# Optimization experiments

Measured on AMD Instinct MI355X. Metric: run time of the kernel, lower is better.

## Reference

```python
import jax, jax.numpy as jnp
import numpy as np

# Marching-tetrahedra lookup tables (identical to the torch module).
_TRI_TABLE = np.array([
    [-1,-1,-1,-1,-1,-1],[1,0,2,-1,-1,-1],[4,0,3,-1,-1,-1],[1,4,2,1,3,4],
    [3,1,5,-1,-1,-1],[2,3,0,2,5,3],[1,4,0,1,5,4],[4,2,5,-1,-1,-1],
    [4,5,2,-1,-1,-1],[4,1,0,4,5,1],[3,2,0,3,5,2],[1,3,5,-1,-1,-1],
    [4,1,2,4,3,1],[3,0,4,-1,-1,-1],[2,0,1,-1,-1,-1],[-1,-1,-1,-1,-1,-1]], dtype=np.int64)
_NUM_TRI = np.array([0,1,1,2,1,2,2,1,1,2,2,1,2,1,1,0], dtype=np.int64)
_BASE_EDGES = np.array([0,1,0,2,0,3,1,2,1,3,2,3], dtype=np.int64)
_NUM_TETS = np.array([0,1,1,3,1,3,3,3,1,3,3,3,3,3,3,1], dtype=np.int64)
_TET_TABLE = np.array([
    [-1,-1,-1,-1,-1,-1,-1,-1,-1,-1,-1,-1],[0,4,5,6,-1,-1,-1,-1,-1,-1,-1,-1],
    [1,4,8,7,-1,-1,-1,-1,-1,-1,-1,-1],[7,1,8,6,5,1,7,6,5,0,1,6],
    [2,5,7,9,-1,-1,-1,-1,-1,-1,-1,-1],[4,0,6,7,9,0,7,6,7,0,9,2],
    [4,1,9,8,5,1,9,4,5,1,2,9],[6,0,1,2,8,6,1,2,9,6,8,2],
    [3,6,9,8,-1,-1,-1,-1,-1,-1,-1,-1],[5,0,4,8,5,0,8,3,5,8,9,3],
    [1,4,7,3,4,7,6,3,9,6,7,3],[0,1,5,3,5,1,9,3,5,1,7,9],
    [5,2,3,7,3,6,5,8,3,5,7,8],[0,4,7,8,0,3,8,7,0,3,7,2],
    [4,1,2,3,4,3,2,5,4,3,5,6],[0,1,2,3,-1,-1,-1,-1,-1,-1,-1,-1]], dtype=np.int64)


def _precompute(n_verts, sdf, tet, thickness):
    """Integer / no_grad half of DMTet.__call__ (dynamic shapes -> host numpy)."""
    sdf = np.asarray(sdf)
    tet = np.asarray(tet).astype(np.int64)
    th = float(np.asarray(thickness).reshape(-1)[0])
    occ = (sdf > 0) & (sdf <= th)                      # [N]
    occ_f = occ[tet]                                   # [F,4]
    occ_sum = occ_f.sum(-1)
    valid = (occ_sum > 0) & (occ_sum < 4)
    vt = tet[valid]                                    # [V,4] surface tets
    edges = vt[:, _BASE_EDGES].reshape(-1, 2)          # [V*6,2]
    edges = np.sort(edges, axis=1)                     # == sort_edges
    uniq, inv = np.unique(edges, axis=0, return_inverse=True)
    inv = inv.reshape(-1)
    mask_e = occ[uniq].sum(-1) == 1                    # crossing edges
    mapping = np.full(uniq.shape[0], -1, dtype=np.int64)
    mapping[mask_e] = np.arange(int(mask_e.sum()), dtype=np.int64)
    idx_map = mapping[inv].reshape(-1, 6)              # [V,6]
    interp_v = uniq[mask_e]                            # [E,2]
    ti = (occ_f[valid].astype(np.int64) * np.array([1, 2, 4, 8])).sum(-1)  # tetindex
    nt = _NUM_TRI[ti]
    f1 = np.take_along_axis(idx_map[nt == 1], _TRI_TABLE[ti[nt == 1]][:, :3], axis=1).reshape(-1, 3)
    f2 = np.take_along_axis(idx_map[nt == 2], _TRI_TABLE[ti[nt == 2]][:, :6], axis=1).reshape(-1, 3)
    faces = np.concatenate([f1, f2], axis=0)
    ntt = _NUM_TETS[ti]
    tve = np.concatenate([vt, idx_map + n_verts], axis=1)  # [V,10]: 4 verts + 6 edge-verts
    t1 = np.take_along_axis(tve[ntt == 1], _TET_TABLE[ti[ntt == 1]][:, :4], axis=1).reshape(-1, 4)
    t3 = np.take_along_axis(tve[ntt == 3], _TET_TABLE[ti[ntt == 3]][:, :12], axis=1).reshape(-1, 4)
    inner = tet[occ_sum == 4]
    all_tets = np.concatenate([t1, t3, inner], axis=0)
    all_unique, inv2 = np.unique(all_tets.reshape(-1), return_inverse=True)
    tets_tetmesh = inv2.reshape(-1, 4)
    return interp_v, faces, all_unique, tets_tetmesh


def _interp(pos, sdf, th, interp_v, all_unique_tets):
    """Differentiable half: edge interpolation + gather of tetmesh verts."""
    e = pos[interp_v.reshape(-1)].reshape(-1, 2, 3)    # [E,2,3]
    s = sdf[interp_v.reshape(-1)].reshape(-1, 2, 1)    # [E,2,1]
    both_pos = (s[:, 0, 0] > 0) & (s[:, 1, 0] > 0)
    s = jnp.where(both_pos[:, None, None], s - th, s)  # shift band edges
    s = s * jnp.array([1.0, -1.0], dtype=s.dtype)[None, :, None]  # negate 2nd
    denom = s.sum(axis=1, keepdims=True)
    w = jnp.flip(s, axis=1) / denom                    # linear interp weights
    verts = (e * w).sum(axis=1)                        # [E,3]
    all_verts = jnp.concatenate([pos, verts], axis=0)
    verts_tetmesh = all_verts[all_unique_tets]
    return verts, verts_tetmesh


def setup_inputs() -> dict:
    key = jax.random.key(0)
    k1, k2, k3, k4 = jax.random.split(key, 4)
    N, F = 400000, 2000000
    pos_nx3 = jax.random.normal(k1, (N, 3), dtype=jnp.float32)
    sdf_n = jax.random.normal(k2, (N,), dtype=jnp.float32)
    tet_fx4 = jax.random.randint(k3, (F, 4), 0, N, dtype=jnp.int32)
    thickness = jax.random.uniform(k4, (1,), dtype=jnp.float32, minval=0.3, maxval=0.8)
    return {"pos_nx3": pos_nx3, "sdf_n": sdf_n, "tet_fx4": tet_fx4, "thickness": thickness}


def reference(pos_nx3, sdf_n, tet_fx4, thickness):
    interp_v, faces, all_unique, tets_tm = _precompute(pos_nx3.shape[0], sdf_n, tet_fx4, thickness)
    verts, verts_tetmesh = _interp(pos_nx3, sdf_n, thickness[0], jnp.asarray(interp_v), jnp.asarray(all_unique))
    return verts, jnp.asarray(faces), verts_tetmesh, jnp.asarray(tets_tm)
```

## Files before the change

kernel.cpp:

```cpp
#include <hip/hip_runtime.h>
#include <stdint.h>

typedef unsigned int u32;
typedef unsigned long long u64;

__device__ __constant__ int c_TRI[16][6] = {
 {-1,-1,-1,-1,-1,-1},{1,0,2,-1,-1,-1},{4,0,3,-1,-1,-1},{1,4,2,1,3,4},
 {3,1,5,-1,-1,-1},{2,3,0,2,5,3},{1,4,0,1,5,4},{4,2,5,-1,-1,-1},
 {4,5,2,-1,-1,-1},{4,1,0,4,5,1},{3,2,0,3,5,2},{1,3,5,-1,-1,-1},
 {4,1,2,4,3,1},{3,0,4,-1,-1,-1},{2,0,1,-1,-1,-1},{-1,-1,-1,-1,-1,-1}};
__device__ __constant__ int c_NTRI[16] = {0,1,1,2,1,2,2,1,1,2,2,1,2,1,1,0};
__device__ __constant__ int c_NTET[16] = {0,1,1,3,1,3,3,3,1,3,3,3,3,3,3,1};
__device__ __constant__ int c_TET[16][12] = {
 {-1,-1,-1,-1,-1,-1,-1,-1,-1,-1,-1,-1},{0,4,5,6,-1,-1,-1,-1,-1,-1,-1,-1},
 {1,4,8,7,-1,-1,-1,-1,-1,-1,-1,-1},{7,1,8,6,5,1,7,6,5,0,1,6},
 {2,5,7,9,-1,-1,-1,-1,-1,-1,-1,-1},{4,0,6,7,9,0,7,6,7,0,9,2},
 {4,1,9,8,5,1,9,4,5,1,2,9},{6,0,1,2,8,6,1,2,9,6,8,2},
 {3,6,9,8,-1,-1,-1,-1,-1,-1,-1,-1},{5,0,4,8,5,0,8,3,5,8,9,3},
 {1,4,7,3,4,7,6,3,9,6,7,3},{0,1,5,3,5,1,9,3,5,1,7,9},
 {5,2,3,7,3,6,5,8,3,5,7,8},{0,4,7,8,0,3,8,7,0,3,7,2},
 {4,1,2,3,4,3,2,5,4,3,5,6},{0,1,2,3,-1,-1,-1,-1,-1,-1,-1,-1}};
__device__ __constant__ int c_EV[12] = {0,1,0,2,0,3,1,2,1,3,2,3};

#define GSLOOP(i,n) for (long long i = (long long)blockIdx.x*blockDim.x + threadIdx.x; \
                         i < (long long)(n); i += (long long)gridDim.x*blockDim.x)

__global__ __launch_bounds__(256) void k_scan1(u32* data, u32* partials,
                                               const u32* hdr, int nslot, u32 nmax) {
  __shared__ u32 lds[2048];
  __shared__ u32 tsum[256];
  u32 n = (nslot >= 0) ? hdr[nslot] : nmax;
  u32 base = blockIdx.x * 2048u;
  for (int k = threadIdx.x; k < 2048; k += 256) {
    u32 i = base + (u32)k;
    lds[k] = (i < n) ? data[i] : 0u;
  }
  __syncthreads();
  u32 o = threadIdx.x * 8u;
  u32 run = 0; u32 loc[8];
  #pragma unroll
  for (int j = 0; j < 8; j++) { loc[j] = run; run += lds[o + j]; }
  tsum[threadIdx.x] = run;
  __syncthreads();
  for (int off = 1; off < 256; off <<= 1) {
    u32 v = tsum[threadIdx.x];
    u32 add = (threadIdx.x >= (u32)off) ? tsum[threadIdx.x - off] : 0u;
    __syncthreads();
    tsum[threadIdx.x] = v + add;
    __syncthreads();
  }
  u32 texc = (threadIdx.x == 0) ? 0u : tsum[threadIdx.x - 1];
  #pragma unroll
  for (int j = 0; j < 8; j++) {
    u32 i = base + o + (u32)j;
    if (i < n) data[i] = texc + loc[j];
  }
  if (threadIdx.x == 0) partials[blockIdx.x] = tsum[255];
}

__global__ __launch_bounds__(1024) void k_scan2(u32* partials, const u32* hdr, int nslot,
                                                u32 nmax, u32* hdrw, int tslot) {
  __shared__ u32 lds[8192];
  __shared__ u32 tsum[1024];
  u32 n = (nslot >= 0) ? hdr[nslot] : nmax;
  u32 nb = (n + 2047u) / 2048u;
  for (int k = threadIdx.x; k < 8192; k += 1024) lds[k] = ((u32)k < nb) ? partials[k] : 0u;
  __syncthreads();
  u32 o = threadIdx.x * 8u;
  u32 run = 0; u32 loc[8];
  #pragma unroll
  for (int j = 0; j < 8; j++) { loc[j] = run; run += lds[o + j]; }
  tsum[threadIdx.x] = run;
  __syncthreads();
  for (int off = 1; off < 1024; off <<= 1) {
    u32 v = tsum[threadIdx.x];
    u32 add = (threadIdx.x >= (u32)off) ? tsum[threadIdx.x - off] : 0u;
    __syncthreads();
    tsum[threadIdx.x] = v + add;
    __syncthreads();
  }
  u32 texc = (threadIdx.x == 0) ? 0u : tsum[threadIdx.x - 1];
  #pragma unroll
  for (int j = 0; j < 8; j++) { u32 k = o + (u32)j; if (k < nb) partials[k] = texc + loc[j]; }
  if (threadIdx.x == 0 && tslot >= 0) hdrw[tslot] = tsum[1023];
}

__global__ __launch_bounds__(256) void k_scan3(u32* data, const u32* partials,
                                               const u32* hdr, int nslot, u32 nmax) {
  u32 n = (nslot >= 0) ? hdr[nslot] : nmax;
  u32 base = blockIdx.x * 2048u;
  if (base >= n || blockIdx.x == 0) return;
  u32 add = partials[blockIdx.x];
  if (add == 0) return;
  for (int k = threadIdx.x; k < 2048; k += 256) {
    u32 i = base + (u32)k;
    if (i < n) data[i] += add;
  }
}

__global__ void k_zero32(u32* p, long long n) { GSLOOP(i, n) p[i] = 0u; }
__global__ void k_zero_hdr(u32* p, const u32* hdr, int slot, u32 extra) {
  long long n = (long long)hdr[slot] + extra;
  GSLOOP(i, n) p[i] = 0u;
}
__global__ void k_copy32(const u32* s, u32* d, long long n) { GSLOOP(i, n) d[i] = s[i]; }

__global__ void k_occ(const float* sdf, const float* th, unsigned char* occ, int N) {
  float t = th[0];
  GSLOOP(i, N) { float s = sdf[i]; occ[i] = (s > 0.f && s <= t) ? 1 : 0; }
}

__global__ void k_ti(const int* tet, const unsigned char* occ, unsigned char* ti,
                     u32* S1, long long F) {
  GSLOOP(f, F) {
    int v0 = tet[4*f], v1 = tet[4*f+1], v2 = tet[4*f+2], v3 = tet[4*f+3];
    int b = (int)occ[v0] | ((int)occ[v1] << 1) | ((int)occ[v2] << 2) | ((int)occ[v3] << 3);
    ti[f] = (unsigned char)b;
    S1[f] = (b != 0 && b != 15) ? 1u : 0u;
  }
}

__global__ void k_compact_valid(const u32* S1, const unsigned char* ti, u32* vidx, long long F) {
  GSLOOP(f, F) { int b = ti[f]; if (b != 0 && b != 15) vidx[S1[f]] = (u32)f; }
}

__global__ void k_hist(const int* tet, const u32* vidx, const u32* hdr, u32* hist) {
  u32 V = hdr[0];
  GSLOOP(t, V) {
    long long f = vidx[t];
    int v[4] = { tet[4*f], tet[4*f+1], tet[4*f+2], tet[4*f+3] };
    #pragma unroll
    for (int e = 0; e < 6; e++) {
      int a = v[c_EV[2*e]], b = v[c_EV[2*e+1]];
      int mn = a < b ? a : b;
      atomicAdd(&hist[mn], 1u);
    }
  }
}

__global__ void k_scatter(const int* tet, const u32* vidx, const u32* hdr,
                          u32* cursor, u64* keys, int SB, int OB) {
  u32 V = hdr[0];
  GSLOOP(t, V) {
    long long f = vidx[t];
    int v[4] = { tet[4*f], tet[4*f+1], tet[4*f+2], tet[4*f+3] };
    #pragma unroll
    for (int e = 0; e < 6; e++) {
      int a = v[c_EV[2*e]], b = v[c_EV[2*e+1]];
      int mn = a < b ? a : b, mx = a < b ? b : a;
      u32 p = atomicAdd(&cursor[mn], 1u);
      u64 key = ((((u64)(u32)mn << SB) | (u64)(u32)mx) << OB) | (u64)(6ull * t + e);
      keys[p] = key;
    }
  }
}

template<int KMAX>
__device__ __forceinline__ void bitonic_lane(u64& val, int lane) {
  #pragma unroll
  for (int k = 2; k <= KMAX; k <<= 1) {
    #pragma unroll
    for (int j = k >> 1; j > 0; j >>= 1) {
      u64 other = __shfl_xor(val, j, 64);
      bool keepmin = ((lane & k) == 0) == ((lane & j) == 0);
      bool smaller = val < other;
      val = (keepmin == smaller) ? val : other;
    }
  }
}

__global__ __launch_bounds__(256) void k_bsort(const u32* off, u64* keys, int N) {
  int lane = threadIdx.x & 63;
  long long wid = ((long long)blockIdx.x * blockDim.x + threadIdx.x) >> 6;
  long long nw  = ((long long)gridDim.x * blockDim.x) >> 6;
  for (long long v = wid; v < N; v += nw) {
    u32 s = off[v], e = off[v + 1];
    u32 cnt = e - s;
    if (cnt <= 1) continue;
    if (cnt <= 64) {
      u64 val = (lane < (int)cnt) ? keys[s + lane] : ~0ull;
      if      (cnt <= 2)  bitonic_lane<2>(val, lane);
      else if (cnt <= 4)  bitonic_lane<4>(val, lane);
      else if (cnt <= 8)  bitonic_lane<8>(val, lane);
      else if (cnt <= 16) bitonic_lane<16>(val, lane);
      else if (cnt <= 32) bitonic_lane<32>(val, lane);
      else                bitonic_lane<64>(val, lane);
      if (lane < (int)cnt) keys[s + lane] = val;
    } else if (cnt <= 256) {
      u64 vals[4];
      #pragma unroll
      for (int r = 0; r < 4; r++) {
        int idx = r * 64 + lane;
        vals[r] = (idx < (int)cnt) ? keys[s + idx] : ~0ull;
      }
      #pragma unroll
      for (int k = 2; k <= 256; k <<= 1) {
        #pragma unroll
        for (int j = 128; j > 0; j >>= 1) {
          if (j >= k) continue;
          if (j >= 64) {
            int rj = j >> 6;
            #pragma unroll
            for (int r = 0; r < 4; r++) {
              int pr = r ^ rj;
              if (pr > r) {
                int i0 = r * 64 + lane;
                bool keepmin = ((i0 & k) == 0);
                u64 a = vals[r], b = vals[pr];
                u64 mn = a < b ? a : b, mx = a < b ? b : a;
                vals[r]  = keepmin ? mn : mx;
                vals[pr] = keepmin ? mx : mn;
              }
            }
          } else {
            #pragma unroll
            for (int r = 0; r < 4; r++) {
              int i0 = r * 64 + lane;
              u64 other = __shfl_xor(vals[r], j, 64);
              bool keepmin = ((i0 & k) == 0) == ((i0 & j) == 0);
              bool smaller = vals[r] < other;
              vals[r] = (keepmin == smaller) ? vals[r] : other;
            }
          }
        }
      }
      #pragma unroll
      for (int r = 0; r < 4; r++) {
        int idx = r * 64 + lane;
        if (idx < (int)cnt) keys[s + idx] = vals[r];
      }
    } else if (lane == 0) {
      for (u32 i = s + 1; i < e; i++) {
        u64 kk = keys[i]; u32 j = i;
        while (j > s && keys[j - 1] > kk) { keys[j] = keys[j - 1]; j--; }
        keys[j] = kk;
      }
    }
  }
}

__global__ void k_uflag(const u64* keys, u32* Big, const u32* hdr, int OB) {
  u32 E = hdr[1];
  GSLOOP(i, E) Big[i] = (i == 0 || (keys[i] >> OB) != (keys[i - 1] >> OB)) ? 1u : 0u;
}

__global__ void k_ucompact(const u64* keys, const u32* Big, u64* uk, const u32* hdr, int OB) {
  u32 E = hdr[1];
  GSLOOP(i, E) {
    u64 k = keys[i] >> OB;
    if (i == 0 || k != (keys[i - 1] >> OB)) uk[Big[i]] = k;
  }
}

__global__ void k_cflag(const u64* uk, const unsigned char* occ, u32* Cf, const u32* hdr, int SB) {
  u32 U = hdr[2];
  u64 mask = ((u64)1 << SB) - 1;
  GSLOOP(u, U) {
    u64 k = uk[u]; int a = (int)(k >> SB), b = (int)(k & mask);
    Cf[u] = (((int)occ[a] + (int)occ[b]) == 1) ? 1u : 0u;
  }
}

__global__ void k_mapping(const u64* uk, const unsigned char* occ, int* Cf,
                          u32* hdr, int N, int SB) {
  if (blockIdx.x == 0 && threadIdx.x == 0) hdr[10] = (u32)N + hdr[3];
  u32 U = hdr[2];
  u64 mask = ((u64)1 << SB) - 1;
  GSLOOP(u, U) {
    u64 k = uk[u]; int a = (int)(k >> SB), b = (int)(k & mask);
    bool c = (((int)occ[a] + (int)occ[b]) == 1);
    Cf[u] = c ? Cf[u] : -1;
  }
}

__global__ void k_idxscatter(const u64* keys, const u32* Big, const int* mapping,
                             int* idx_map, const u32* hdr, int OB) {
  u32 E = hdr[1];
  u64 omask = ((u64)1 << OB) - 1;
  GSLOOP(i, E) {
    u64 k = keys[i];
    bool flag = (i == 0) || ((k >> OB) != (keys[i - 1] >> OB));
    u32 rank = flag ? Big[i] : Big[i] - 1u;
    idx_map[(u32)(k & omask)] = mapping[rank];
  }
}

__global__ void k_interp(const u64* uk, const int* mapping, const float* pos,
                         const float* sdf, const float* th, float* out, const u32* hdr, int SB) {
  u32 U = hdr[2];
  float t = th[0];
  u64 mask = ((u64)1 << SB) - 1;
  GSLOOP(u, U) {
    int m = mapping[u]; if (m < 0) continue;
    u64 k = uk[u]; int a = (int)(k >> SB), b = (int)(k & mask);
    float s0 = sdf[a], s1 = sdf[b];
    if (s0 > 0.f && s1 > 0.f) { s0 = __fsub_rn(s0, t); s1 = __fsub_rn(s1, t); }
    float denom = __fadd_rn(s0, -s1);
    float w0 = __fdiv_rn(-s1, denom);
    float w1 = __fdiv_rn(s0, denom);
    long long base = 3ll * m;
    #pragma unroll
    for (int kk = 0; kk < 3; kk++)
      out[base + kk] = __fadd_rn(__fmul_rn(pos[3ll*a + kk], w0), __fmul_rn(pos[3ll*b + kk], w1));
  }
}

__global__ void k_pred_faces(const unsigned char* ti, u32* S1, u32* S2, long long F) {
  GSLOOP(f, F) {
    int b = ti[f]; bool valid = (b != 0 && b != 15); int nt = c_NTRI[b];
    S1[f] = (valid && nt == 1) ? 1u : 0u;
    S2[f] = (valid && nt == 2) ? 1u : 0u;
  }
}

__global__ void k_faces(const u32* vidx, const unsigned char* ti, const int* idx_map,
                        const u32* S1, const u32* S2, float* out, const u32* hdr) {
  u32 V = hdr[0];
  unsigned long long fo = 3ull * hdr[3];
  u32 Nf1 = hdr[4];
  GSLOOP(t, V) {
    u32 f = vidx[t]; int b = ti[f]; int nt = c_NTRI[b];
    if (nt == 1) {
      unsigned long long base = fo + 3ull * S1[f];
      for (int k = 0; k < 3; k++) out[base + k] = (float)idx_map[6*t + c_TRI[b][k]];
    } else {
      unsigned long long base = fo + 3ull * Nf1 + 6ull * S2[f];
      for (int k = 0; k < 6; k++) out[base + k] = (float)idx_map[6*t + c_TRI[b][k]];
    }
  }
}

__global__ void k_pred_tets(const unsigned char* ti, u32* S1, u32* S2, u32* S3, long long F) {
  GSLOOP(f, F) {
    int b = ti[f]; bool valid = (b != 0 && b != 15); int ntt = c_NTET[b];
    S1[f] = (valid && ntt == 1) ? 1u : 0u;
    S2[f] = (valid && ntt == 3) ? 1u : 0u;
    S3[f] = (b == 15) ? 1u : 0u;
  }
}

__global__ void k_tets_valid(const int* tet, const u32* vidx, const unsigned char* ti,
                             const int* idx_map, const u32* S1, const u32* S2,
                             int* at, const u32* hdr, int N) {
  u32 V = hdr[0]; u32 Nt1 = hdr[6];
  GSLOOP(t, V) {
    u32 f = vidx[t]; int b = ti[f];
    int tv[10];
    for (int k = 0; k < 4; k++) tv[k] = tet[4ll*f + k];
    for (int j = 0; j < 6; j++) tv[4 + j] = idx_map[6*t + j] + N;
    int ntt = c_NTET[b];
    if (ntt == 1) {
      long long base = 4ll * S1[f];
      for (int k = 0; k < 4; k++) at[base + k] = tv[c_TET[b][k]];
    } else {
      long long base = 4ll * Nt1 + 12ll * S2[f];
      for (int k = 0; k < 12; k++) at[base + k] = tv[c_TET[b][k]];
    }
  }
}

__global__ void k_tets_inner(const int* tet, const unsigned char* ti, const u32* S3,
                             int* at, const u32* hdr, long long F) {
  long long base0 = 4ll * hdr[6] + 12ll * hdr[7];
  GSLOOP(f, F) {
    if (ti[f] == 15) {
      long long base = base0 + 4ll * S3[f];
      for (int k = 0; k < 4; k++) at[base + k] = tet[4*f + k];
    }
  }
}

__global__ void k_mark(const int* at, u32* Big, const u32* hdr) {
  long long NA = 4ll * hdr[6] + 12ll * hdr[7] + 4ll * hdr[8];
  GSLOOP(i, NA) Big[at[i]] = 1u;
}

__global__ void k_vtm(const u32* Big, const float* pos, float* out, const u32* hdr, int N) {
  u32 R = hdr[10], NU = hdr[9];
  unsigned long long vtm = 3ull * hdr[3] + 3ull * (hdr[4] + 2u * hdr[5]);
  GSLOOP(v, R) {
    u32 r = Big[v];
    u32 nx = (v + 1 < (long long)R) ? Big[v + 1] : NU;
    if (nx > r) {
      unsigned long long base = vtm + 3ull * r;
      if (v < N) { for (int k = 0; k < 3; k++) out[base + k] = pos[3*v + k]; }
      else { long long src = 3ll * (v - N); for (int k = 0; k < 3; k++) out[base + k] = out[src + k]; }
    }
  }
}

__global__ void k_tets_out(const int* at, const u32* Big, float* out, const u32* hdr) {
  long long NA = 4ll * hdr[6] + 12ll * hdr[7] + 4ll * hdr[8];
  unsigned long long toff = 3ull * hdr[3] + 3ull * (hdr[4] + 2u * hdr[5]) + 3ull * hdr[9];
  GSLOOP(i, NA) out[toff + i] = (float)Big[at[i]];
}

extern "C" void kernel_launch(void* const* d_in, const int* in_sizes, int n_in,
                              void* d_out, int out_size, void* d_ws, size_t ws_size,
                              hipStream_t stream) {
  const float* pos = (const float*)d_in[0];
  const float* sdf = (const float*)d_in[1];
  const int*   tet = (const int*)d_in[2];
  const float* th  = (const float*)d_in[3];
  float* out = (float*)d_out;

  const int N = in_sizes[1];
  const long long F = (long long)in_sizes[2] / 4;
  const long long MAXE = 6 * F;
  const long long RMAX = (long long)N + MAXE;
  (void)n_in; (void)out_size; (void)ws_size;

  int SB = 1; while ((1ll << SB) < (long long)N) SB++;
  int OB = 1; while ((1ll << OB) < MAXE) OB++;

  char* w = (char*)d_ws;
  size_t off = 0;
  auto alloc = [&](size_t b) -> char* {
    char* p = w + off; off = (off + b + 255) & ~(size_t)255; return p;
  };
  u32* hdr            = (u32*)alloc(64 * 4);
  unsigned char* occ  = (unsigned char*)alloc((size_t)N);
  unsigned char* tiA  = (unsigned char*)alloc((size_t)F);
  u32* S1             = (u32*)alloc(4 * (size_t)F);
  u32* S2             = (u32*)alloc(4 * (size_t)F);
  u32* S3             = (u32*)alloc(4 * (size_t)F);
  u32* vidx           = (u32*)alloc(4 * (size_t)F);
  u32* hist           = (u32*)alloc(4 * ((size_t)N + 2));
  u32* cursor         = (u32*)alloc(4 * ((size_t)N + 2));
  void* keys_mem      = alloc(8 * (size_t)MAXE);
  u64* keys = (u64*)keys_mem; int* at = (int*)keys_mem;
  u64* uk             = (u64*)alloc(8 * (size_t)MAXE);
  u32* Big            = (u32*)alloc(4 * ((size_t)RMAX + 2));
  int* mapping        = (int*)alloc(4 * (size_t)MAXE);
  int* idx_map        = (int*)alloc(4 * (size_t)MAXE);
  u32* partials       = (u32*)alloc(4 * 8192);

  const int GRID = 4096, BLK = 256;
  auto scan = [&](u32* data, int nslot, u32 nmax, int tslot) {
    int nb = (int)((nmax + 2047u) / 2048u);
    k_scan1<<<nb, 256, 0, stream>>>(data, partials, hdr, nslot, nmax);
    k_scan2<<<1, 1024, 0, stream>>>(partials, hdr, nslot, nmax, hdr, tslot);
    k_scan3<<<nb, 256, 0, stream>>>(data, partials, hdr, nslot, nmax);
  };

  k_zero32<<<1, 64, 0, stream>>>(hdr, 64);
  k_zero32<<<2048, BLK, 0, stream>>>(hist, (long long)N + 2);

  k_occ<<<GRID, BLK, 0, stream>>>(sdf, th, occ, N);
  k_ti<<<GRID, BLK, 0, stream>>>(tet, occ, tiA, S1, F);
  scan(S1, -1, (u32)F, 0);
  k_compact_valid<<<GRID, BLK, 0, stream>>>(S1, tiA, vidx, F);

  k_hist<<<GRID, BLK, 0, stream>>>(tet, vidx, hdr, hist);
  scan(hist, -1, (u32)(N + 1), 1);
  k_copy32<<<GRID, BLK, 0, stream>>>(hist, cursor, (long long)N + 2);
  k_scatter<<<GRID, BLK, 0, stream>>>(tet, vidx, hdr, cursor, keys, SB, OB);
  k_bsort<<<GRID, BLK, 0, stream>>>(hist, keys, N);

  k_uflag<<<GRID, BLK, 0, stream>>>(keys, Big, hdr, OB);
  scan(Big, 1, (u32)MAXE, 2);
  k_ucompact<<<GRID, BLK, 0, stream>>>(keys, Big, uk, hdr, OB);

  k_cflag<<<GRID, BLK, 0, stream>>>(uk, occ, (u32*)mapping, hdr, SB);
  scan((u32*)mapping, 2, (u32)MAXE, 3);
  k_mapping<<<GRID, BLK, 0, stream>>>(uk, occ, mapping, hdr, N, SB);
  k_idxscatter<<<GRID, BLK, 0, stream>>>(keys, Big, mapping, idx_map, hdr, OB);

  k_interp<<<GRID, BLK, 0, stream>>>(uk, mapping, pos, sdf, th, out, hdr, SB);

  k_pred_faces<<<GRID, BLK, 0, stream>>>(tiA, S1, S2, F);
  scan(S1, -1, (u32)F, 4);
  scan(S2, -1, (u32)F, 5);
  k_faces<<<GRID, BLK, 0, stream>>>(vidx, tiA, idx_map, S1, S2, out, hdr);

  k_pred_tets<<<GRID, BLK, 0, stream>>>(tiA, S1, S2, S3, F);
  scan(S1, -1, (u32)F, 6);
  scan(S2, -1, (u32)F, 7);
  scan(S3, -1, (u32)F, 8);
  k_tets_valid<<<GRID, BLK, 0, stream>>>(tet, vidx, tiA, idx_map, S1, S2, at, hdr, N);
  k_tets_inner<<<GRID, BLK, 0, stream>>>(tet, tiA, S3, at, hdr, F);

  k_zero_hdr<<<GRID, BLK, 0, stream>>>(Big, hdr, 10, 2u);
  k_mark<<<GRID, BLK, 0, stream>>>(at, Big, hdr);
  scan(Big, 10, (u32)RMAX, 9);
  k_vtm<<<GRID, BLK, 0, stream>>>(Big, pos, out, hdr, N);
  k_tets_out<<<GRID, BLK, 0, stream>>>(at, Big, out, hdr);
}
```

Before: 1.768 ms.

## Sort 32-bit max-vertex keys per bucket and rebuild idx_map via binary search

Edge keys shrink from 64-bit packed (min,max,origin) to 32-bit max-vertex values stored in per-min-vertex buckets. The sort now also emits unique flags, which removes the uflag pass. idx_map is rebuilt by a binary search inside each bucket's unique range instead of scattering original edge ids. The scatter is split into 8 min-vertex ranges so atomics and writes stay localized, at the cost of every block rereading all tets 8 times.

New measurement: 2.248 ms. +27.2%, slower.

```diff
diff --git a/kernel.cpp b/kernel.cpp
--- a/kernel.cpp
+++ b/kernel.cpp
@@ -138,30 +138,44 @@
   }
 }
 
-__global__ void k_scatter(const int* tet, const u32* vidx, const u32* hdr,
-                          u32* cursor, u64* keys, int SB, int OB) {
+__global__ void k_bnd(const u32* off, u32* hdr, int N) {
+  int g = threadIdx.x;
+  if (g > 8) return;
+  if (g == 8) { hdr[16 + 8] = (u32)N; return; }
+  u64 target = ((u64)hdr[1] * (u64)g) / 8ull;
+  u32 lo = 0, hi = (u32)N;
+  while (lo < hi) { u32 m = (lo + hi) >> 1; if ((u64)off[m] < target) lo = m + 1; else hi = m; }
+  hdr[16 + g] = lo;
+}
+
+__global__ void k_scatter8(const int* tet, const u32* vidx, const u32* hdr,
+                           u32* cursor, u32* bmx) {
+  int g = blockIdx.x & 7;
+  u32 lo = hdr[16 + g], hi = hdr[16 + g + 1];
   u32 V = hdr[0];
-  GSLOOP(t, V) {
+  for (long long t = (long long)(blockIdx.x >> 3) * blockDim.x + threadIdx.x; t < (long long)V;
+       t += (long long)(gridDim.x >> 3) * blockDim.x) {
     long long f = vidx[t];
     int v[4] = { tet[4*f], tet[4*f+1], tet[4*f+2], tet[4*f+3] };
     #pragma unroll
     for (int e = 0; e < 6; e++) {
       int a = v[c_EV[2*e]], b = v[c_EV[2*e+1]];
       int mn = a < b ? a : b, mx = a < b ? b : a;
-      u32 p = atomicAdd(&cursor[mn], 1u);
-      u64 key = ((((u64)(u32)mn << SB) | (u64)(u32)mx) << OB) | (u64)(6ull * t + e);
-      keys[p] = key;
+      if ((u32)mn >= lo && (u32)mn < hi) {
+        u32 p = atomicAdd(&cursor[mn], 1u);
+        bmx[p] = (u32)mx;
+      }
     }
   }
 }
 
 template<int KMAX>
-__device__ __forceinline__ void bitonic_lane(u64& val, int lane) {
+__device__ __forceinline__ void bitonic_lane(u32& val, int lane) {
   #pragma unroll
   for (int k = 2; k <= KMAX; k <<= 1) {
     #pragma unroll
     for (int j = k >> 1; j > 0; j >>= 1) {
-      u64 other = __shfl_xor(val, j, 64);
+      u32 other = __shfl_xor(val, j, 64);
       bool keepmin = ((lane & k) == 0) == ((lane & j) == 0);
       bool smaller = val < other;
       val = (keepmin == smaller) ? val : other;
@@ -169,29 +183,34 @@
   }
 }
 
-__global__ __launch_bounds__(256) void k_bsort(const u32* off, u64* keys, int N) {
+__global__ __launch_bounds__(256) void k_bsort(const u32* off, u32* bmx, u32* Fl, int N) {
   int lane = threadIdx.x & 63;
   long long wid = ((long long)blockIdx.x * blockDim.x + threadIdx.x) >> 6;
   long long nw  = ((long long)gridDim.x * blockDim.x) >> 6;
   for (long long v = wid; v < N; v += nw) {
     u32 s = off[v], e = off[v + 1];
     u32 cnt = e - s;
-    if (cnt <= 1) continue;
+    if (cnt == 0) continue;
+    if (cnt == 1) { if (lane == 0) Fl[s] = 1u; continue; }
     if (cnt <= 64) {
-      u64 val = (lane < (int)cnt) ? keys[s + lane] : ~0ull;
+      u32 val = (lane < (int)cnt) ? bmx[s + lane] : 0xffffffffu;
       if      (cnt <= 2)  bitonic_lane<2>(val, lane);
       else if (cnt <= 4)  bitonic_lane<4>(val, lane);
       else if (cnt <= 8)  bitonic_lane<8>(val, lane);
       else if (cnt <= 16) bitonic_lane<16>(val, lane);
       else if (cnt <= 32) bitonic_lane<32>(val, lane);
       else                bitonic_lane<64>(val, lane);
-      if (lane < (int)cnt) keys[s + lane] = val;
+      u32 prev = __shfl_up(val, 1, 64);
+      if (lane < (int)cnt) {
+        bmx[s + lane] = val;
+        Fl[s + lane] = (lane == 0 || val != prev) ? 1u : 0u;
+      }
     } else if (cnt <= 256) {
-      u64 vals[4];
+      u32 vals[4];
       #pragma unroll
       for (int r = 0; r < 4; r++) {
         int idx = r * 64 + lane;
-        vals[r] = (idx < (int)cnt) ? keys[s + idx] : ~0ull;
+        vals[r] = (idx < (int)cnt) ? bmx[s + idx] : 0xffffffffu;
       }
       #pragma unroll
       for (int k = 2; k <= 256; k <<= 1) {
@@ -206,8 +225,8 @@
               if (pr > r) {
                 int i0 = r * 64 + lane;
                 bool keepmin = ((i0 & k) == 0);
-                u64 a = vals[r], b = vals[pr];
-                u64 mn = a < b ? a : b, mx = a < b ? b : a;
+                u32 a = vals[r], b = vals[pr];
+                u32 mn = a < b ? a : b, mx = a < b ? b : a;
                 vals[r]  = keepmin ? mn : mx;
                 vals[pr] = keepmin ? mx : mn;
               }
@@ -216,7 +235,7 @@
             #pragma unroll
             for (int r = 0; r < 4; r++) {
               int i0 = r * 64 + lane;
-              u64 other = __shfl_xor(vals[r], j, 64);
+              u32 other = __shfl_xor(vals[r], j, 64);
               bool keepmin = ((i0 & k) == 0) == ((i0 & j) == 0);
               bool smaller = vals[r] < other;
               vals[r] = (keepmin == smaller) ? vals[r] : other;
@@ -226,73 +245,90 @@
       }
       #pragma unroll
       for (int r = 0; r < 4; r++) {
+        u32 pv = __shfl_up(vals[r], 1, 64);
+        u32 lastprev = (r > 0) ? __shfl(vals[r - 1], 63, 64) : 0u;
         int idx = r * 64 + lane;
-        if (idx < (int)cnt) keys[s + idx] = vals[r];
+        u32 prev = (lane == 0) ? lastprev : pv;
+        if (idx < (int)cnt) {
+          bmx[s + idx] = vals[r];
+          Fl[s + idx] = (idx == 0 || vals[r] != prev) ? 1u : 0u;
+        }
       }
     } else if (lane == 0) {
       for (u32 i = s + 1; i < e; i++) {
-        u64 kk = keys[i]; u32 j = i;
-        while (j > s && keys[j - 1] > kk) { keys[j] = keys[j - 1]; j--; }
-        keys[j] = kk;
-      }
-    }
-  }
-}
-
-__global__ void k_uflag(const u64* keys, u32* Big, const u32* hdr, int OB) {
-  u32 E = hdr[1];
-  GSLOOP(i, E) Big[i] = (i == 0 || (keys[i] >> OB) != (keys[i - 1] >> OB)) ? 1u : 0u;
-}
-
-__global__ void k_ucompact(const u64* keys, const u32* Big, u64* uk, const u32* hdr, int OB) {
-  u32 E = hdr[1];
-  GSLOOP(i, E) {
-    u64 k = keys[i] >> OB;
-    if (i == 0 || k != (keys[i - 1] >> OB)) uk[Big[i]] = k;
-  }
-}
-
-__global__ void k_cflag(const u64* uk, const unsigned char* occ, u32* Cf, const u32* hdr, int SB) {
+        u32 kk = bmx[i]; u32 j = i;
+        while (j > s && bmx[j - 1] > kk) { bmx[j] = bmx[j - 1]; j--; }
+        bmx[j] = kk;
+      }
+      for (u32 j = s; j < e; j++) Fl[j] = (j == s || bmx[j] != bmx[j - 1]) ? 1u : 0u;
+    }
+  }
+}
+
+__global__ __launch_bounds__(256) void k_ucompact(const u32* off, const u32* bmx,
+                                                  const u32* Rk, u64* uk, int N) {
+  int lane = threadIdx.x & 63;
+  long long wid = ((long long)blockIdx.x * blockDim.x + threadIdx.x) >> 6;
+  long long nw  = ((long long)gridDim.x * blockDim.x) >> 6;
+  for (long long v = wid; v < N; v += nw) {
+    u32 s = off[v], e = off[v + 1];
+    for (u32 j = s + (u32)lane; j < e; j += 64) {
+      u32 mx = bmx[j];
+      bool fl = (j == s) || (mx != bmx[j - 1]);
+      if (fl) uk[Rk[j]] = ((u64)v << 32) | (u64)mx;
+    }
+  }
+}
+
+__global__ void k_cflag(const u64* uk, const unsigned char* occ, u32* Cf, const u32* hdr) {
   u32 U = hdr[2];
-  u64 mask = ((u64)1 << SB) - 1;
   GSLOOP(u, U) {
-    u64 k = uk[u]; int a = (int)(k >> SB), b = (int)(k & mask);
+    u64 k = uk[u]; int a = (int)(k >> 32), b = (int)(k & 0xffffffffu);
     Cf[u] = (((int)occ[a] + (int)occ[b]) == 1) ? 1u : 0u;
   }
 }
 
 __global__ void k_mapping(const u64* uk, const unsigned char* occ, int* Cf,
-                          u32* hdr, int N, int SB) {
+                          u32* hdr, int N) {
   if (blockIdx.x == 0 && threadIdx.x == 0) hdr[10] = (u32)N + hdr[3];
   u32 U = hdr[2];
-  u64 mask = ((u64)1 << SB) - 1;
   GSLOOP(u, U) {
-    u64 k = uk[u]; int a = (int)(k >> SB), b = (int)(k & mask);
+    u64 k = uk[u]; int a = (int)(k >> 32), b = (int)(k & 0xffffffffu);
     bool c = (((int)occ[a] + (int)occ[b]) == 1);
     Cf[u] = c ? Cf[u] : -1;
   }
 }
 
-__global__ void k_idxscatter(const u64* keys, const u32* Big, const int* mapping,
-                             int* idx_map, const u32* hdr, int OB) {
-  u32 E = hdr[1];
-  u64 omask = ((u64)1 << OB) - 1;
-  GSLOOP(i, E) {
-    u64 k = keys[i];
-    bool flag = (i == 0) || ((k >> OB) != (keys[i - 1] >> OB));
-    u32 rank = flag ? Big[i] : Big[i] - 1u;
-    idx_map[(u32)(k & omask)] = mapping[rank];
+__global__ void k_idxmap(const int* tet, const u32* vidx, const u32* off,
+                         const u32* Rk, const u64* uk, const int* mapping,
+                         int* idx_map, const u32* hdr) {
+  u32 V = hdr[0], E = hdr[1], U = hdr[2];
+  GSLOOP(t, V) {
+    long long f = vidx[t];
+    int v[4] = { tet[4*f], tet[4*f+1], tet[4*f+2], tet[4*f+3] };
+    #pragma unroll
+    for (int e = 0; e < 6; e++) {
+      int a = v[c_EV[2*e]], b = v[c_EV[2*e+1]];
+      int mn = a < b ? a : b, mx = a < b ? b : a;
+      u32 s = off[mn], s2 = off[mn + 1];
+      u32 lo = Rk[s];
+      u32 hi = (s2 < E) ? Rk[s2] : U;
+      while (lo < hi) {
+        u32 m = (lo + hi) >> 1;
+        if ((u32)(uk[m] & 0xffffffffu) < (u32)mx) lo = m + 1; else hi = m;
+      }
+      idx_map[6 * t + e] = mapping[lo];
+    }
   }
 }
 
 __global__ void k_interp(const u64* uk, const int* mapping, const float* pos,
-                         const float* sdf, const float* th, float* out, const u32* hdr, int SB) {
+                         const float* sdf, const float* th, float* out, const u32* hdr) {
   u32 U = hdr[2];
   float t = th[0];
-  u64 mask = ((u64)1 << SB) - 1;
   GSLOOP(u, U) {
     int m = mapping[u]; if (m < 0) continue;
-    u64 k = uk[u]; int a = (int)(k >> SB), b = (int)(k & mask);
+    u64 k = uk[u]; int a = (int)(k >> 32), b = (int)(k & 0xffffffffu);
     float s0 = sdf[a], s1 = sdf[b];
     if (s0 > 0.f && s1 > 0.f) { s0 = __fsub_rn(s0, t); s1 = __fsub_rn(s1, t); }
     float denom = __fadd_rn(s0, -s1);
@@ -410,9 +446,6 @@
   const long long RMAX = (long long)N + MAXE;
   (void)n_in; (void)out_size; (void)ws_size;
 
-  int SB = 1; while ((1ll << SB) < (long long)N) SB++;
-  int OB = 1; while ((1ll << OB) < MAXE) OB++;
-
   char* w = (char*)d_ws;
   size_t off = 0;
   auto alloc = [&](size_t b) -> char* {
@@ -427,8 +460,10 @@
   u32* vidx           = (u32*)alloc(4 * (size_t)F);
   u32* hist           = (u32*)alloc(4 * ((size_t)N + 2));
   u32* cursor         = (u32*)alloc(4 * ((size_t)N + 2));
-  void* keys_mem      = alloc(8 * (size_t)MAXE);
-  u64* keys = (u64*)keys_mem; int* at = (int*)keys_mem;
+  char* big_mem       = alloc(8 * (size_t)MAXE);
+  u32* bmx = (u32*)big_mem;
+  u32* Rk  = (u32*)(big_mem + 4 * (size_t)MAXE);
+  int* at  = (int*)big_mem;
   u64* uk             = (u64*)alloc(8 * (size_t)MAXE);
   u32* Big            = (u32*)alloc(4 * ((size_t)RMAX + 2));
   int* mapping        = (int*)alloc(4 * (size_t)MAXE);
@@ -453,20 +488,20 @@
 
   k_hist<<<GRID, BLK, 0, stream>>>(tet, vidx, hdr, hist);
   scan(hist, -1, (u32)(N + 1), 1);
+  k_bnd<<<1, 64, 0, stream>>>(hist, hdr, N);
   k_copy32<<<GRID, BLK, 0, stream>>>(hist, cursor, (long long)N + 2);
-  k_scatter<<<GRID, BLK, 0, stream>>>(tet, vidx, hdr, cursor, keys, SB, OB);
-  k_bsort<<<GRID, BLK, 0, stream>>>(hist, keys, N);
-
-  k_uflag<<<GRID, BLK, 0, stream>>>(keys, Big, hdr, OB);
-  scan(Big, 1, (u32)MAXE, 2);
-  k_ucompact<<<GRID, BLK, 0, stream>>>(keys, Big, uk, hdr, OB);
-
-  k_cflag<<<GRID, BLK, 0, stream>>>(uk, occ, (u32*)mapping, hdr, SB);
+  k_scatter8<<<GRID, BLK, 0, stream>>>(tet, vidx, hdr, cursor, bmx);
+  k_bsort<<<GRID, BLK, 0, stream>>>(hist, bmx, Rk, N);
+
+  scan(Rk, 1, (u32)MAXE, 2);
+  k_ucompact<<<GRID, BLK, 0, stream>>>(hist, bmx, Rk, uk, N);
+
+  k_cflag<<<GRID, BLK, 0, stream>>>(uk, occ, (u32*)mapping, hdr);
   scan((u32*)mapping, 2, (u32)MAXE, 3);
-  k_mapping<<<GRID, BLK, 0, stream>>>(uk, occ, mapping, hdr, N, SB);
-  k_idxscatter<<<GRID, BLK, 0, stream>>>(keys, Big, mapping, idx_map, hdr, OB);
-
-  k_interp<<<GRID, BLK, 0, stream>>>(uk, mapping, pos, sdf, th, out, hdr, SB);
+  k_mapping<<<GRID, BLK, 0, stream>>>(uk, occ, mapping, hdr, N);
+  k_idxmap<<<GRID, BLK, 0, stream>>>(tet, vidx, hist, Rk, uk, mapping, idx_map, hdr);
+
+  k_interp<<<GRID, BLK, 0, stream>>>(uk, mapping, pos, sdf, th, out, hdr);
 
   k_pred_faces<<<GRID, BLK, 0, stream>>>(tiA, S1, S2, F);
   scan(S1, -1, (u32)F, 4);
```

## Fuse unique/crossing flags into bucket sort and partition scatter by key range

Applied to the files above, without the earlier changes.

The per-bucket sort now also computes each sorted key's unique-edge and crossing flags. This removes the separate uflag, ucompact, cflag and mapping kernels along with one full-length scan and the uk array. Scatter and idx_map writes are split into 8 range slices, so each block group writes only a contiguous region, which is meant to improve write locality. The cost is that every block group reads all tets/keys and filters them, so the read and compute work is repeated about 8 times.

Measured after the change: 1.622 ms. -8.2%, faster.

```diff
diff --git a/kernel.cpp b/kernel.cpp
--- a/kernel.cpp
+++ b/kernel.cpp
@@ -104,6 +104,7 @@
   GSLOOP(i, n) p[i] = 0u;
 }
 __global__ void k_copy32(const u32* s, u32* d, long long n) { GSLOOP(i, n) d[i] = s[i]; }
+__global__ void k_setr(u32* hdr, int N) { hdr[10] = (u32)N + hdr[3]; }
 
 __global__ void k_occ(const float* sdf, const float* th, unsigned char* occ, int N) {
   float t = th[0];
@@ -138,19 +139,33 @@
   }
 }
 
-__global__ void k_scatter(const int* tet, const u32* vidx, const u32* hdr,
-                          u32* cursor, u64* keys, int SB, int OB) {
+__global__ void k_bnd(const u32* off, u32* hdr, int N) {
+  int g = threadIdx.x;
+  if (g > 8) return;
+  if (g == 8) { hdr[16 + 8] = (u32)N; return; }
+  u64 target = ((u64)hdr[1] * (u64)g) / 8ull;
+  u32 lo = 0, hi = (u32)N;
+  while (lo < hi) { u32 m = (lo + hi) >> 1; if ((u64)off[m] < target) lo = m + 1; else hi = m; }
+  hdr[16 + g] = lo;
+}
+
+__global__ void k_scatter8(const int* tet, const u32* vidx, const u32* hdr,
+                           u32* cursor, u64* keys, int SB, int OB) {
+  int g = blockIdx.x & 7;
+  u32 lo = hdr[16 + g], hi = hdr[16 + g + 1];
   u32 V = hdr[0];
-  GSLOOP(t, V) {
+  for (long long t = (long long)(blockIdx.x >> 3) * blockDim.x + threadIdx.x; t < (long long)V;
+       t += (long long)(gridDim.x >> 3) * blockDim.x) {
     long long f = vidx[t];
     int v[4] = { tet[4*f], tet[4*f+1], tet[4*f+2], tet[4*f+3] };
     #pragma unroll
     for (int e = 0; e < 6; e++) {
       int a = v[c_EV[2*e]], b = v[c_EV[2*e+1]];
       int mn = a < b ? a : b, mx = a < b ? b : a;
-      u32 p = atomicAdd(&cursor[mn], 1u);
-      u64 key = ((((u64)(u32)mn << SB) | (u64)(u32)mx) << OB) | (u64)(6ull * t + e);
-      keys[p] = key;
+      if ((u32)mn >= lo && (u32)mn < hi) {
+        u32 p = atomicAdd(&cursor[mn], 1u);
+        keys[p] = (((u64)(u32)mn << (SB + OB)) | ((u64)(u32)mx << OB)) | (u64)(6ull * t + e);
+      }
     }
   }
 }
@@ -169,14 +184,25 @@
   }
 }
 
-__global__ __launch_bounds__(256) void k_bsort(const u32* off, u64* keys, int N) {
+__global__ __launch_bounds__(256) void k_bsort(const u32* off, u64* keys, u32* cfe,
+                                               const unsigned char* occm, int N,
+                                               int SB, int OB) {
   int lane = threadIdx.x & 63;
+  u64 smask = ((u64)1 << SB) - 1;
   long long wid = ((long long)blockIdx.x * blockDim.x + threadIdx.x) >> 6;
   long long nw  = ((long long)gridDim.x * blockDim.x) >> 6;
   for (long long v = wid; v < N; v += nw) {
     u32 s = off[v], e = off[v + 1];
     u32 cnt = e - s;
-    if (cnt <= 1) continue;
+    if (cnt == 0) continue;
+    int ov = (int)occm[v];
+    if (cnt == 1) {
+      if (lane == 0) {
+        u32 mx = (u32)((keys[s] >> OB) & smask);
+        cfe[s] = ((ov + (int)occm[mx]) == 1) ? 1u : 0u;
+      }
+      continue;
+    }
     if (cnt <= 64) {
       u64 val = (lane < (int)cnt) ? keys[s + lane] : ~0ull;
       if      (cnt <= 2)  bitonic_lane<2>(val, lane);
@@ -185,7 +211,13 @@
       else if (cnt <= 16) bitonic_lane<16>(val, lane);
       else if (cnt <= 32) bitonic_lane<32>(val, lane);
       else                bitonic_lane<64>(val, lane);
-      if (lane < (int)cnt) keys[s + lane] = val;
+      u64 prev = __shfl_up(val, 1, 64);
+      if (lane < (int)cnt) {
+        keys[s + lane] = val;
+        bool flag = (lane == 0) || ((val >> OB) != (prev >> OB));
+        u32 mx = (u32)((val >> OB) & smask);
+        cfe[s + lane] = (flag && ((ov + (int)occm[mx]) == 1)) ? 1u : 0u;
+      }
     } else if (cnt <= 256) {
       u64 vals[4];
       #pragma unroll
@@ -226,8 +258,16 @@
       }
       #pragma unroll
       for (int r = 0; r < 4; r++) {
+        u64 pv = __shfl_up(vals[r], 1, 64);
+        u64 lastprev = (r > 0) ? __shfl(vals[r - 1], 63, 64) : 0ull;
         int idx = r * 64 + lane;
-        if (idx < (int)cnt) keys[s + idx] = vals[r];
+        u64 prev = (lane == 0) ? lastprev : pv;
+        if (idx < (int)cnt) {
+          keys[s + idx] = vals[r];
+          bool flag = (idx == 0) || ((vals[r] >> OB) != (prev >> OB));
+          u32 mx = (u32)((vals[r] >> OB) & smask);
+          cfe[s + idx] = (flag && ((ov + (int)occm[mx]) == 1)) ? 1u : 0u;
+        }
       }
     } else if (lane == 0) {
       for (u32 i = s + 1; i < e; i++) {
@@ -235,64 +275,43 @@
         while (j > s && keys[j - 1] > kk) { keys[j] = keys[j - 1]; j--; }
         keys[j] = kk;
       }
-    }
-  }
-}
-
-__global__ void k_uflag(const u64* keys, u32* Big, const u32* hdr, int OB) {
+      for (u32 j = s; j < e; j++) {
+        bool flag = (j == s) || ((keys[j] >> OB) != (keys[j - 1] >> OB));
+        u32 mx = (u32)((keys[j] >> OB) & smask);
+        cfe[j] = (flag && ((ov + (int)occm[mx]) == 1)) ? 1u : 0u;
+      }
+    }
+  }
+}
+
+__global__ void k_idxscatter8(const u64* keys, const u32* S, const unsigned char* occm,
+                              int* idx_map, u64* ie, const u32* hdr, int SB, int OB) {
   u32 E = hdr[1];
-  GSLOOP(i, E) Big[i] = (i == 0 || (keys[i] >> OB) != (keys[i - 1] >> OB)) ? 1u : 0u;
-}
-
-__global__ void k_ucompact(const u64* keys, const u32* Big, u64* uk, const u32* hdr, int OB) {
-  u32 E = hdr[1];
-  GSLOOP(i, E) {
-    u64 k = keys[i] >> OB;
-    if (i == 0 || k != (keys[i - 1] >> OB)) uk[Big[i]] = k;
-  }
-}
-
-__global__ void k_cflag(const u64* uk, const unsigned char* occ, u32* Cf, const u32* hdr, int SB) {
-  u32 U = hdr[2];
-  u64 mask = ((u64)1 << SB) - 1;
-  GSLOOP(u, U) {
-    u64 k = uk[u]; int a = (int)(k >> SB), b = (int)(k & mask);
-    Cf[u] = (((int)occ[a] + (int)occ[b]) == 1) ? 1u : 0u;
-  }
-}
-
-__global__ void k_mapping(const u64* uk, const unsigned char* occ, int* Cf,
-                          u32* hdr, int N, int SB) {
-  if (blockIdx.x == 0 && threadIdx.x == 0) hdr[10] = (u32)N + hdr[3];
-  u32 U = hdr[2];
-  u64 mask = ((u64)1 << SB) - 1;
-  GSLOOP(u, U) {
-    u64 k = uk[u]; int a = (int)(k >> SB), b = (int)(k & mask);
-    bool c = (((int)occ[a] + (int)occ[b]) == 1);
-    Cf[u] = c ? Cf[u] : -1;
-  }
-}
-
-__global__ void k_idxscatter(const u64* keys, const u32* Big, const int* mapping,
-                             int* idx_map, const u32* hdr, int OB) {
-  u32 E = hdr[1];
+  int g = blockIdx.x & 7;
   u64 omask = ((u64)1 << OB) - 1;
-  GSLOOP(i, E) {
+  u64 smask = ((u64)1 << SB) - 1;
+  for (long long i = (long long)(blockIdx.x >> 3) * blockDim.x + threadIdx.x; i < (long long)E;
+       i += (long long)(gridDim.x >> 3) * blockDim.x) {
     u64 k = keys[i];
+    u32 oidx = (u32)(k & omask);
+    u32 mx = (u32)((k >> OB) & smask);
+    u32 mn = (u32)(k >> (SB + OB));
     bool flag = (i == 0) || ((k >> OB) != (keys[i - 1] >> OB));
-    u32 rank = flag ? Big[i] : Big[i] - 1u;
-    idx_map[(u32)(k & omask)] = mapping[rank];
-  }
-}
-
-__global__ void k_interp(const u64* uk, const int* mapping, const float* pos,
-                         const float* sdf, const float* th, float* out, const u32* hdr, int SB) {
-  u32 U = hdr[2];
+    bool cf = ((int)occm[mn] + (int)occm[mx]) == 1;
+    u32 sv = S[i];
+    int mapval = cf ? (int)(flag ? sv : sv - 1u) : -1;
+    u32 slice = (u32)(((u64)oidx * 8ull) / (u64)E);
+    if (slice == (u32)g) idx_map[oidx] = mapval;
+    if (g == 0 && flag && cf) ie[sv] = ((u64)mn << 32) | (u64)mx;
+  }
+}
+
+__global__ void k_interp(const u64* ie, const float* pos, const float* sdf,
+                         const float* th, float* out, const u32* hdr) {
+  u32 EC = hdr[3];
   float t = th[0];
-  u64 mask = ((u64)1 << SB) - 1;
-  GSLOOP(u, U) {
-    int m = mapping[u]; if (m < 0) continue;
-    u64 k = uk[u]; int a = (int)(k >> SB), b = (int)(k & mask);
+  GSLOOP(m, EC) {
+    u64 k = ie[m]; int a = (int)(k >> 32), b = (int)(k & 0xffffffffu);
     float s0 = sdf[a], s1 = sdf[b];
     if (s0 > 0.f && s1 > 0.f) { s0 = __fsub_rn(s0, t); s1 = __fsub_rn(s1, t); }
     float denom = __fadd_rn(s0, -s1);
@@ -427,11 +446,11 @@
   u32* vidx           = (u32*)alloc(4 * (size_t)F);
   u32* hist           = (u32*)alloc(4 * ((size_t)N + 2));
   u32* cursor         = (u32*)alloc(4 * ((size_t)N + 2));
-  void* keys_mem      = alloc(8 * (size_t)MAXE);
-  u64* keys = (u64*)keys_mem; int* at = (int*)keys_mem;
-  u64* uk             = (u64*)alloc(8 * (size_t)MAXE);
+  char* big_mem       = alloc(8 * (size_t)MAXE);
+  u64* keys = (u64*)big_mem; int* at = (int*)big_mem;
+  u64* ie             = (u64*)alloc(8 * (size_t)MAXE);
   u32* Big            = (u32*)alloc(4 * ((size_t)RMAX + 2));
-  int* mapping        = (int*)alloc(4 * (size_t)MAXE);
+  u32* cfe            = (u32*)alloc(4 * (size_t)MAXE);
   int* idx_map        = (int*)alloc(4 * (size_t)MAXE);
   u32* partials       = (u32*)alloc(4 * 8192);
 
@@ -453,20 +472,16 @@
 
   k_hist<<<GRID, BLK, 0, stream>>>(tet, vidx, hdr, hist);
   scan(hist, -1, (u32)(N + 1), 1);
+  k_bnd<<<1, 64, 0, stream>>>(hist, hdr, N);
   k_copy32<<<GRID, BLK, 0, stream>>>(hist, cursor, (long long)N + 2);
-  k_scatter<<<GRID, BLK, 0, stream>>>(tet, vidx, hdr, cursor, keys, SB, OB);
-  k_bsort<<<GRID, BLK, 0, stream>>>(hist, keys, N);
-
-  k_uflag<<<GRID, BLK, 0, stream>>>(keys, Big, hdr, OB);
-  scan(Big, 1, (u32)MAXE, 2);
-  k_ucompact<<<GRID, BLK, 0, stream>>>(keys, Big, uk, hdr, OB);
-
-  k_cflag<<<GRID, BLK, 0, stream>>>(uk, occ, (u32*)mapping, hdr, SB);
-  scan((u32*)mapping, 2, (u32)MAXE, 3);
-  k_mapping<<<GRID, BLK, 0, stream>>>(uk, occ, mapping, hdr, N, SB);
-  k_idxscatter<<<GRID, BLK, 0, stream>>>(keys, Big, mapping, idx_map, hdr, OB);
-
-  k_interp<<<GRID, BLK, 0, stream>>>(uk, mapping, pos, sdf, th, out, hdr, SB);
+  k_scatter8<<<GRID, BLK, 0, stream>>>(tet, vidx, hdr, cursor, keys, SB, OB);
+  k_bsort<<<GRID, BLK, 0, stream>>>(hist, keys, cfe, occ, N, SB, OB);
+
+  scan(cfe, 1, (u32)MAXE, 3);
+  k_setr<<<1, 1, 0, stream>>>(hdr, N);
+  k_idxscatter8<<<GRID, BLK, 0, stream>>>(keys, cfe, occ, idx_map, ie, hdr, SB, OB);
+
+  k_interp<<<GRID, BLK, 0, stream>>>(ie, pos, sdf, th, out, hdr);
 
   k_pred_faces<<<GRID, BLK, 0, stream>>>(tiA, S1, S2, F);
   scan(S1, -1, (u32)F, 4);
```
